# Kernel tuning notes

Measured on AMD Instinct MI355X. Metric: run time of the kernel, lower is better.

## Reference

```python
import jax, jax.numpy as jnp
import numpy as np

K = 100  # low-rank dimension


def setup_inputs() -> dict:
    key = jax.random.key(0)
    k1, k2 = jax.random.split(key)
    N, D = 100000, 512
    X = jax.random.normal(k1, (N, D), dtype=jnp.float32)
    # xavier-normal init for Linear(d, 4k): std = sqrt(2/(fan_in+fan_out))
    std = np.sqrt(2.0 / (D + 4 * K)).astype(np.float32)
    W = jax.random.normal(k2, (4 * K, D), dtype=jnp.float32) * std
    b = jnp.zeros((4 * K,), dtype=jnp.float32)
    return {"X": X, "W": W, "b": b}


def reference(X, W, b):
    # tmp = ReLU(X @ W^T + b): [N, 4k]
    tmp = jax.nn.relu(X @ W.T + b)
    U = tmp[:, :K]            # [N, k]
    V = tmp[:, K:2 * K]       # [N, k]
    Z = tmp[:, 2 * K:3 * K]   # [N, k]
    T = tmp[:, 3 * K:]        # [N, k]
    N_rows = X.shape[0]
    # joint_normalize2: sum(U @ (V^T @ ones)) / N + 1e-6 == <colsum(U), colsum(V)> / N + 1e-6
    norm_factor = jnp.dot(jnp.sum(U, axis=0), jnp.sum(V, axis=0)) / N_rows + 1e-6
    Dscale = 1.0 / norm_factor
    # low-rank attention: U @ (V^T @ Z) via small [k, k] intermediate
    VtZ = jnp.einsum('nk,nj->kj', V, Z)   # [k, k]
    res = (U @ VtZ) * Dscale              # [N, k]
    out = jnp.concatenate([res, T], axis=1)  # [N, 2k]
    # dropout p=0.0 (eval-equivalent): identity
    return out
```

## Files before the change

### kernel.cpp

```cpp
#include <hip/hip_runtime.h>
#include <cstdint>

typedef __bf16 bf16;
typedef __attribute__((ext_vector_type(8))) __bf16 bf16x8;
typedef __attribute__((ext_vector_type(4))) __bf16 bf16x4;
typedef __attribute__((ext_vector_type(4))) float f32x4;

#define NROWS 100000
#define DIM   512
#define NC    400
#define NBLK2 782

#define WS_WP    0u
#define WS_SUMU  458752u
#define WS_SUMV  459152u
#define WS_DSC   459552u
#define WS_VTZT  459776u
#define WS_U     524288u
#define WS_PART  66124288u
#define WS_SUMP  71041536u
#define WS_NEED  71667136u

__device__ __forceinline__ void gload_lds16(const void* g, void* l) {
  __builtin_amdgcn_global_load_lds(
      (const __attribute__((address_space(1))) uint32_t*)g,
      (__attribute__((address_space(3))) uint32_t*)l,
      16, 0, 0);
}

__global__ void k1_prep(const float* __restrict__ W, bf16* __restrict__ wp,
                        float* __restrict__ sums) {
  const int idx = blockIdx.x * 256 + threadIdx.x;
  if (idx < 200) sums[idx] = 0.f;
  if (idx >= 16 * 4 * 448 * 8) return;
  const int e = idx & 7;
  int r = idx >> 3;
  const int col = r % 448; r /= 448;
  const int g = r & 3;
  const int t = r >> 2;
  const int k = t * 32 + 4 * g + ((e < 4) ? e : (12 + e));
  wp[idx] = (bf16)((col < NC) ? W[col * DIM + k] : 0.f);
}

__global__ __launch_bounds__(512, 2) void k2_main(
    const float* __restrict__ X, const bf16* __restrict__ Wp,
    const float* __restrict__ bias, float* __restrict__ out,
    bf16* __restrict__ U, float* __restrict__ part, float* __restrict__ sumP) {
  __shared__ __align__(16) char pool[106496];
  char* Abase0 = pool;
  char* Bbase0 = pool + 49152;

  const int tid  = threadIdx.x;
  const int lane = tid & 63;
  const int wave = tid >> 6;
  const int wm = wave >> 2;
  const int wn = wave & 3;
  const int m  = lane & 15;
  const int g  = lane >> 4;
  const int rb = blockIdx.x * 128;

  f32x4 acc[4][7];
#pragma unroll
  for (int i = 0; i < 4; ++i)
#pragma unroll
    for (int j = 0; j < 7; ++j) acc[i][j] = (f32x4){0.f, 0.f, 0.f, 0.f};

  int gr0 = rb + wave * 16 + (lane >> 3);     if (gr0 > NROWS - 1) gr0 = NROWS - 1;
  int gr1 = rb + wave * 16 + 8 + (lane >> 3); if (gr1 > NROWS - 1) gr1 = NROWS - 1;
  const size_t swb = (size_t)(((lane & 7) ^ (lane >> 3)) * 16);
  const char* asrc0 = (const char*)X + (size_t)gr0 * 2048 + swb;
  const char* asrc1 = (const char*)X + (size_t)gr1 * 2048 + swb;
  const int bc0 = (wave < 4) ? wave * 4 : 16 + (wave - 4) * 3;
  const int nbc = (wave < 4) ? 4 : 3;
  const char* wpc = (const char*)Wp;

#define STAGE_A(T, BUF)                                                        \
  do {                                                                         \
    char* ad = Abase0 + (BUF) * 16384 + wave * 2048 + lane * 16;               \
    gload_lds16(asrc0 + (size_t)(T) * 128, ad);                                \
    gload_lds16(asrc1 + (size_t)(T) * 128, ad + 1024);                         \
  } while (0)
#define STAGE_B(T, BUF)                                                        \
  do {                                                                         \
    const char* bsrc = wpc + (size_t)(T) * 28672;                              \
    for (int q = 0; q < nbc; ++q)                                              \
      gload_lds16(bsrc + (bc0 + q) * 1024 + lane * 16,                         \
                  Bbase0 + (BUF) * 28672 + (bc0 + q) * 1024);                  \
  } while (0)

  STAGE_A(0, 0);
  STAGE_B(0, 0);
  STAGE_A(1, 1);

#pragma unroll
  for (int t = 0; t < 16; ++t) {
    const int ab  = t % 3;
    const int bb_ = t & 1;
    if (t < 15) STAGE_B(t + 1, bb_ ^ 1);
    if (t < 14) STAGE_A(t + 2, (t + 2) % 3);
    if (t < 14) {
      if (wave < 4) asm volatile("s_waitcnt vmcnt(8)\n\ts_barrier" ::: "memory");
      else          asm volatile("s_waitcnt vmcnt(7)\n\ts_barrier" ::: "memory");
    } else if (t == 14) {
      if (wave < 4) asm volatile("s_waitcnt vmcnt(6)\n\ts_barrier" ::: "memory");
      else          asm volatile("s_waitcnt vmcnt(5)\n\ts_barrier" ::: "memory");
    } else {
      asm volatile("s_waitcnt vmcnt(0)\n\ts_barrier" ::: "memory");
    }

    const int sw = (m & 7) * 16;
    const char* abuf = Abase0 + ab * 16384;
    bf16x8 af[4];
#pragma unroll
    for (int mf = 0; mf < 4; ++mf) {
      const char* rowp = abuf + (wm * 64 + mf * 16 + m) * 128;
      f32x4 alo = *(const f32x4*)(rowp + ((16 * g) ^ sw));
      f32x4 ahi = *(const f32x4*)(rowp + ((64 + 16 * g) ^ sw));
      af[mf] = (bf16x8){(bf16)alo.x, (bf16)alo.y, (bf16)alo.z, (bf16)alo.w,
                        (bf16)ahi.x, (bf16)ahi.y, (bf16)ahi.z, (bf16)ahi.w};
    }

    const bf16* Bc = (const bf16*)(Bbase0 + bb_ * 28672);
#pragma unroll
    for (int nf = 0; nf < 7; ++nf) {
      const int n = wn * 112 + nf * 16 + m;
      bf16x8 bfr = *(const bf16x8*)(Bc + (g * 448 + n) * 8);
#pragma unroll
      for (int mf = 0; mf < 4; ++mf)
        acc[mf][nf] = __builtin_amdgcn_mfma_f32_16x16x32_bf16(af[mf], bfr, acc[mf][nf], 0, 0, 0);
    }
    asm volatile("s_barrier" ::: "memory");
  }
#undef STAGE_A
#undef STAGE_B

  bf16* ldsVZ = (bf16*)pool;
  float* sp   = (float*)(pool + 61440);
  float csum[7];
#pragma unroll
  for (int nf = 0; nf < 7; ++nf) csum[nf] = 0.f;

#pragma unroll
  for (int mf = 0; mf < 4; ++mf) {
#pragma unroll
    for (int nf = 0; nf < 7; ++nf) {
      const int c = wn * 112 + nf * 16 + m;
      const float bv = (c < NC) ? bias[c] : 0.f;
#pragma unroll
      for (int r = 0; r < 4; ++r) {
        const int rl = wm * 64 + mf * 16 + 4 * g + r;
        const int row = rb + rl;
        float v = fmaxf(acc[mf][nf][r] + bv, 0.f);
        const float v2 = (row < NROWS) ? v : 0.f;
        if (row < NROWS) {
          if (c < 128) U[(size_t)row * 128 + c] = (c < 100) ? (bf16)v : (bf16)0.f;
          if (c >= 300 && c < NC) out[(size_t)row * 200 + 100 + (c - 300)] = v;
        }
        if (c >= 100 && c < 300)
          ldsVZ[(size_t)((c < 200) ? (c - 100) : (112 + (c - 200))) * 136 + rl] = (bf16)v2;
        if (c < 200) csum[nf] += v2;
      }
    }
  }
  for (int i = tid; i < 3264; i += 512) {
    const int q = i / 136, off = i % 136;
    const int lrow = (q < 12) ? (100 + q) : (200 + q);
    ldsVZ[lrow * 136 + off] = (bf16)0.f;
  }
#pragma unroll
  for (int nf = 0; nf < 7; ++nf) {
    float s = csum[nf];
    s += __shfl_xor(s, 16, 64);
    s += __shfl_xor(s, 32, 64);
    if (lane < 16) sp[wave * 112 + nf * 16 + lane] = s;
  }
  __syncthreads();

  if (wave < 7) {
    f32x4 acc2[7];
#pragma unroll
    for (int j = 0; j < 7; ++j) acc2[j] = (f32x4){0.f, 0.f, 0.f, 0.f};
    const bf16* vA = ldsVZ + (size_t)(wave * 16 + m) * 136;
#pragma unroll
    for (int kc = 0; kc < 4; ++kc) {
      bf16x4 a0 = *(const bf16x4*)(vA + kc * 32 + 4 * g);
      bf16x4 a1 = *(const bf16x4*)(vA + kc * 32 + 16 + 4 * g);
      bf16x8 af_ = {a0[0], a0[1], a0[2], a0[3], a1[0], a1[1], a1[2], a1[3]};
#pragma unroll
      for (int fj = 0; fj < 7; ++fj) {
        const bf16* vB = ldsVZ + (size_t)(112 + fj * 16 + m) * 136 + kc * 32;
        bf16x4 b0 = *(const bf16x4*)(vB + 4 * g);
        bf16x4 b1 = *(const bf16x4*)(vB + 16 + 4 * g);
        bf16x8 bf_ = {b0[0], b0[1], b0[2], b0[3], b1[0], b1[1], b1[2], b1[3]};
        acc2[fj] = __builtin_amdgcn_mfma_f32_16x16x32_bf16(af_, bf_, acc2[fj], 0, 0, 0);
      }
    }
    float* pb = part + (size_t)(blockIdx.x % 98) * 12544;
#pragma unroll
    for (int fj = 0; fj < 7; ++fj)
#pragma unroll
      for (int r = 0; r < 4; ++r)
        atomicAdd(&pb[(wave * 16 + 4 * g + r) * 112 + fj * 16 + m], acc2[fj][r]);
  }
  if (tid < 200) {
    const int wnc = tid / 112, cc = tid % 112;
    sumP[(size_t)blockIdx.x * 200 + tid] =
        sp[wnc * 112 + cc] + sp[(wnc + 4) * 112 + cc];
  }
}

__global__ void k4a0_redsum(const float* __restrict__ sumP,
                            float* __restrict__ sumU, float* __restrict__ sumV) {
  __shared__ float red[4];
  const int c = blockIdx.x;
  const int tid = threadIdx.x;
  float s = 0.f;
  for (int b = tid; b < NBLK2; b += 256) s += sumP[(size_t)b * 200 + c];
#pragma unroll
  for (int off = 1; off < 64; off <<= 1) s += __shfl_xor(s, off, 64);
  if ((tid & 63) == 0) red[tid >> 6] = s;
  __syncthreads();
  if (tid == 0) {
    float t = red[0] + red[1] + red[2] + red[3];
    if (c < 100) sumU[c] = t; else sumV[c - 100] = t;
  }
}

__global__ void k4a_norm(const float* __restrict__ sumU, const float* __restrict__ sumV,
                         float* __restrict__ dsc) {
  const int l = threadIdx.x;
  float v = 0.f;
  if (l < 50) v = sumU[l] * sumV[l] + sumU[l + 50] * sumV[l + 50];
#pragma unroll
  for (int off = 32; off > 0; off >>= 1) v += __shfl_down(v, off, 64);
  if (l == 0) dsc[0] = 1.f / (v * (1.f / (float)NROWS) + 1e-6f);
}

__global__ void k4b_final(const float* __restrict__ part, const float* __restrict__ dsc,
                          bf16* __restrict__ vtzt) {
  const int idx = blockIdx.x * 256 + threadIdx.x;
  if (idx < 1792) vtzt[(idx >> 4) * 128 + 112 + (idx & 15)] = (bf16)0.f;
  if (idx >= 12544) return;
  const int i = idx / 112;
  const int j = idx % 112;
  float s = 0.f;
#pragma unroll 7
  for (int bb = 0; bb < 98; ++bb) s += part[(size_t)bb * 12544 + idx];
  vtzt[j * 128 + i] = (bf16)(s * dsc[0]);
}

__global__ __launch_bounds__(256) void k5_res(
    const bf16* __restrict__ U, const bf16* __restrict__ vtzt,
    float* __restrict__ out) {
  const int tid = threadIdx.x;
  const int lane = tid & 63;
  const int wave = tid >> 6;
  const int m = lane & 15, g = lane >> 4;
  const int rb = blockIdx.x * 128 + wave * 32;

  f32x4 acc[2][7];
#pragma unroll
  for (int i = 0; i < 2; ++i)
#pragma unroll
    for (int j = 0; j < 7; ++j) acc[i][j] = (f32x4){0.f, 0.f, 0.f, 0.f};

  int r0 = rb + m;      if (r0 > NROWS - 1) r0 = NROWS - 1;
  int r1 = rb + 16 + m; if (r1 > NROWS - 1) r1 = NROWS - 1;
  const bf16* u0 = U + (size_t)r0 * 128 + 4 * g;
  const bf16* u1 = U + (size_t)r1 * 128 + 4 * g;
  const bf16* vb = vtzt + 4 * g;

#pragma unroll
  for (int ks = 0; ks < 4; ++ks) {
    bf16x4 A00 = *(const bf16x4*)(u0 + ks * 32);
    bf16x4 A01 = *(const bf16x4*)(u0 + ks * 32 + 16);
    bf16x4 A10 = *(const bf16x4*)(u1 + ks * 32);
    bf16x4 A11 = *(const bf16x4*)(u1 + ks * 32 + 16);
    bf16x8 af0 = {A00[0], A00[1], A00[2], A00[3], A01[0], A01[1], A01[2], A01[3]};
    bf16x8 af1 = {A10[0], A10[1], A10[2], A10[3], A11[0], A11[1], A11[2], A11[3]};
#pragma unroll
    for (int nf = 0; nf < 7; ++nf) {
      const int n = nf * 16 + m;
      bf16x4 B0 = *(const bf16x4*)(vb + n * 128 + ks * 32);
      bf16x4 B1 = *(const bf16x4*)(vb + n * 128 + ks * 32 + 16);
      bf16x8 bfr = {B0[0], B0[1], B0[2], B0[3], B1[0], B1[1], B1[2], B1[3]};
      acc[0][nf] = __builtin_amdgcn_mfma_f32_16x16x32_bf16(af0, bfr, acc[0][nf], 0, 0, 0);
      acc[1][nf] = __builtin_amdgcn_mfma_f32_16x16x32_bf16(af1, bfr, acc[1][nf], 0, 0, 0);
    }
  }
#pragma unroll
  for (int mf = 0; mf < 2; ++mf)
#pragma unroll
    for (int nf = 0; nf < 7; ++nf)
#pragma unroll
      for (int r = 0; r < 4; ++r) {
        const int row = rb + mf * 16 + 4 * g + r;
        const int c = nf * 16 + m;
        if (row < NROWS && c < 100)
          out[(size_t)row * 200 + c] = acc[mf][nf][r];
      }
}

extern "C" void kernel_launch(void* const* d_in, const int* in_sizes, int n_in,
                              void* d_out, int out_size, void* d_ws, size_t ws_size,
                              hipStream_t stream) {
  const float* X = (const float*)d_in[0];
  const float* W = (const float*)d_in[1];
  const float* b = (const float*)d_in[2];
  float* out = (float*)d_out;
  char* ws = (char*)d_ws;
  if (ws_size < WS_NEED) return;

  bf16* wp     = (bf16*)(ws + WS_WP);
  float* sumU  = (float*)(ws + WS_SUMU);
  float* sumV  = (float*)(ws + WS_SUMV);
  float* dsc   = (float*)(ws + WS_DSC);
  bf16* vtzt   = (bf16*)(ws + WS_VTZT);
  bf16* U      = (bf16*)(ws + WS_U);
  float* part  = (float*)(ws + WS_PART);
  float* sumP  = (float*)(ws + WS_SUMP);

  k1_prep<<<896, 256, 0, stream>>>(W, wp, sumU);
  hipMemsetAsync(part, 0, 98u * 12544u * 4u, stream);
  k2_main<<<NBLK2, 512, 0, stream>>>(X, wp, b, out, U, part, sumP);
  k4a0_redsum<<<200, 256, 0, stream>>>(sumP, sumU, sumV);
  k4a_norm<<<1, 64, 0, stream>>>(sumU, sumV, dsc);
  k4b_final<<<49, 256, 0, stream>>>(part, dsc, vtzt);
  k5_res<<<782, 256, 0, stream>>>(U, vtzt, out);
}
```

Before: 208.8 us.

## Split rows between LDS-staged kernel and a register-direct 64-row GEMM variant

Half the rows go through the existing LDS-staged 128-row kernel. The other half go through a new kernel that loads X directly into registers, converts it to bf16, and reads packed W fragments from global memory in 64-row blocks. The per-block V^T Z partials are split across two halves of the partial buffer, and the column-sum reduction is extended to cover both launches. The aim is to cut LDS staging overhead and raise occupancy, at the cost of repeated global W reads and an extra kernel launch.

```diff
diff --git a/kernel.cpp b/kernel.cpp
--- a/kernel.cpp
+++ b/kernel.cpp
@@ -9,7 +9,10 @@
 #define NROWS 100000
 #define DIM   512
 #define NC    400
-#define NBLK2 782
+#define NBLK_V0 391
+#define NBLK_V1 781
+#define ROW0_V1 50048
+#define NBLKTOT 1172
 
 #define WS_WP    0u
 #define WS_SUMU  458752u
@@ -19,7 +22,7 @@
 #define WS_U     524288u
 #define WS_PART  66124288u
 #define WS_SUMP  71041536u
-#define WS_NEED  71667136u
+#define WS_NEED  71979136u
 
 __device__ __forceinline__ void gload_lds16(const void* g, void* l) {
   __builtin_amdgcn_global_load_lds(
@@ -42,7 +45,7 @@
   wp[idx] = (bf16)((col < NC) ? W[col * DIM + k] : 0.f);
 }
 
-__global__ __launch_bounds__(512, 2) void k2_main(
+__global__ __launch_bounds__(512, 2) void k2_v0(
     const float* __restrict__ X, const bf16* __restrict__ Wp,
     const float* __restrict__ bias, float* __restrict__ out,
     bf16* __restrict__ U, float* __restrict__ part, float* __restrict__ sumP) {
@@ -195,7 +198,7 @@
         acc2[fj] = __builtin_amdgcn_mfma_f32_16x16x32_bf16(af_, bf_, acc2[fj], 0, 0, 0);
       }
     }
-    float* pb = part + (size_t)(blockIdx.x % 98) * 12544;
+    float* pb = part + (size_t)(blockIdx.x % 49) * 12544;
 #pragma unroll
     for (int fj = 0; fj < 7; ++fj)
 #pragma unroll
@@ -205,6 +208,127 @@
   if (tid < 200) {
     const int wnc = tid / 112, cc = tid % 112;
     sumP[(size_t)blockIdx.x * 200 + tid] =
+        sp[wnc * 112 + cc] + sp[(wnc + 4) * 112 + cc];
+  }
+}
+
+__global__ __launch_bounds__(512) void k2_v1(
+    const float* __restrict__ X, const bf16* __restrict__ Wp,
+    const float* __restrict__ bias, float* __restrict__ out,
+    bf16* __restrict__ U, float* __restrict__ part, float* __restrict__ sumP) {
+  __shared__ __align__(16) bf16 ldsVZ[224 * 72];
+  __shared__ float sp[8 * 112];
+
+  const int tid  = threadIdx.x;
+  const int lane = tid & 63;
+  const int wave = tid >> 6;
+  const int wm = wave >> 2;
+  const int wn = wave & 3;
+  const int m  = lane & 15;
+  const int g  = lane >> 4;
+  const int rbl = blockIdx.x * 64;
+  const int rb  = ROW0_V1 + rbl + wm * 32;
+
+  f32x4 acc[2][7];
+#pragma unroll
+  for (int i = 0; i < 2; ++i)
+#pragma unroll
+    for (int j = 0; j < 7; ++j) acc[i][j] = (f32x4){0.f, 0.f, 0.f, 0.f};
+
+  int r0 = rb + m;      if (r0 > NROWS - 1) r0 = NROWS - 1;
+  int r1 = rb + 16 + m; if (r1 > NROWS - 1) r1 = NROWS - 1;
+  const float* xp0 = X + (size_t)r0 * DIM + 4 * g;
+  const float* xp1 = X + (size_t)r1 * DIM + 4 * g;
+  const char* wb = (const char*)Wp + (size_t)(g * 448 + wn * 112 + m) * 16;
+
+#pragma unroll
+  for (int t = 0; t < 16; ++t) {
+    f32x4 a00 = *(const f32x4*)(xp0 + t * 32);
+    f32x4 a01 = *(const f32x4*)(xp0 + t * 32 + 16);
+    f32x4 a10 = *(const f32x4*)(xp1 + t * 32);
+    f32x4 a11 = *(const f32x4*)(xp1 + t * 32 + 16);
+    bf16x8 af0 = {(bf16)a00.x, (bf16)a00.y, (bf16)a00.z, (bf16)a00.w,
+                  (bf16)a01.x, (bf16)a01.y, (bf16)a01.z, (bf16)a01.w};
+    bf16x8 af1 = {(bf16)a10.x, (bf16)a10.y, (bf16)a10.z, (bf16)a10.w,
+                  (bf16)a11.x, (bf16)a11.y, (bf16)a11.z, (bf16)a11.w};
+    const char* wt = wb + (size_t)t * 28672;
+#pragma unroll
+    for (int nf = 0; nf < 7; ++nf) {
+      bf16x8 bfr = *(const bf16x8*)(wt + nf * 256);
+      acc[0][nf] = __builtin_amdgcn_mfma_f32_16x16x32_bf16(af0, bfr, acc[0][nf], 0, 0, 0);
+      acc[1][nf] = __builtin_amdgcn_mfma_f32_16x16x32_bf16(af1, bfr, acc[1][nf], 0, 0, 0);
+    }
+  }
+
+  float csum[7];
+#pragma unroll
+  for (int nf = 0; nf < 7; ++nf) csum[nf] = 0.f;
+
+#pragma unroll
+  for (int mf = 0; mf < 2; ++mf) {
+#pragma unroll
+    for (int nf = 0; nf < 7; ++nf) {
+      const int c = wn * 112 + nf * 16 + m;
+      const float bv = (c < NC) ? bias[c] : 0.f;
+#pragma unroll
+      for (int r = 0; r < 4; ++r) {
+        const int rl = wm * 32 + mf * 16 + 4 * g + r;
+        const int row = ROW0_V1 + rbl + rl;
+        float v = fmaxf(acc[mf][nf][r] + bv, 0.f);
+        const float v2 = (row < NROWS) ? v : 0.f;
+        if (row < NROWS) {
+          if (c < 128) U[(size_t)row * 128 + c] = (c < 100) ? (bf16)v : (bf16)0.f;
+          if (c >= 300 && c < NC) out[(size_t)row * 200 + 100 + (c - 300)] = v;
+        }
+        if (c >= 100 && c < 300)
+          ldsVZ[(size_t)((c < 200) ? (c - 100) : (112 + (c - 200))) * 72 + rl] = (bf16)v2;
+        if (c < 200) csum[nf] += v2;
+      }
+    }
+  }
+  for (int i = tid; i < 1728; i += 512) {
+    const int q = i / 72, off = i % 72;
+    const int lrow = (q < 12) ? (100 + q) : (200 + q);
+    ldsVZ[lrow * 72 + off] = (bf16)0.f;
+  }
+#pragma unroll
+  for (int nf = 0; nf < 7; ++nf) {
+    float s = csum[nf];
+    s += __shfl_xor(s, 16, 64);
+    s += __shfl_xor(s, 32, 64);
+    if (lane < 16) sp[wave * 112 + nf * 16 + lane] = s;
+  }
+  __syncthreads();
+
+  if (wave < 7) {
+    f32x4 acc2[7];
+#pragma unroll
+    for (int j = 0; j < 7; ++j) acc2[j] = (f32x4){0.f, 0.f, 0.f, 0.f};
+    const bf16* vA = ldsVZ + (size_t)(wave * 16 + m) * 72;
+#pragma unroll
+    for (int kc = 0; kc < 2; ++kc) {
+      bf16x4 a0 = *(const bf16x4*)(vA + kc * 32 + 4 * g);
+      bf16x4 a1 = *(const bf16x4*)(vA + kc * 32 + 16 + 4 * g);
+      bf16x8 af_ = {a0[0], a0[1], a0[2], a0[3], a1[0], a1[1], a1[2], a1[3]};
+#pragma unroll
+      for (int fj = 0; fj < 7; ++fj) {
+        const bf16* vB = ldsVZ + (size_t)(112 + fj * 16 + m) * 72 + kc * 32;
+        bf16x4 b0 = *(const bf16x4*)(vB + 4 * g);
+        bf16x4 b1 = *(const bf16x4*)(vB + 16 + 4 * g);
+        bf16x8 bf_ = {b0[0], b0[1], b0[2], b0[3], b1[0], b1[1], b1[2], b1[3]};
+        acc2[fj] = __builtin_amdgcn_mfma_f32_16x16x32_bf16(af_, bf_, acc2[fj], 0, 0, 0);
+      }
+    }
+    float* pb = part + (size_t)(49 + blockIdx.x % 49) * 12544;
+#pragma unroll
+    for (int fj = 0; fj < 7; ++fj)
+#pragma unroll
+      for (int r = 0; r < 4; ++r)
+        atomicAdd(&pb[(wave * 16 + 4 * g + r) * 112 + fj * 16 + m], acc2[fj][r]);
+  }
+  if (tid < 200) {
+    const int wnc = tid / 112, cc = tid % 112;
+    sumP[(size_t)(NBLK_V0 + blockIdx.x) * 200 + tid] =
         sp[wnc * 112 + cc] + sp[(wnc + 4) * 112 + cc];
   }
 }
@@ -215,7 +339,7 @@
   const int c = blockIdx.x;
   const int tid = threadIdx.x;
   float s = 0.f;
-  for (int b = tid; b < NBLK2; b += 256) s += sumP[(size_t)b * 200 + c];
+  for (int b = tid; b < NBLKTOT; b += 256) s += sumP[(size_t)b * 200 + c];
 #pragma unroll
   for (int off = 1; off < 64; off <<= 1) s += __shfl_xor(s, off, 64);
   if ((tid & 63) == 0) red[tid >> 6] = s;
@@ -322,7 +446,8 @@
 
   k1_prep<<<896, 256, 0, stream>>>(W, wp, sumU);
   hipMemsetAsync(part, 0, 98u * 12544u * 4u, stream);
-  k2_main<<<NBLK2, 512, 0, stream>>>(X, wp, b, out, U, part, sumP);
+  k2_v0<<<NBLK_V0, 512, 0, stream>>>(X, wp, b, out, U, part, sumP);
+  k2_v1<<<NBLK_V1, 512, 0, stream>>>(X, wp, b, out, U, part, sumP);
   k4a0_redsum<<<200, 256, 0, stream>>>(sumP, sumU, sumV);
   k4a_norm<<<1, 64, 0, stream>>>(sumU, sumV, dsc);
   k4b_final<<<49, 256, 0, stream>>>(part, dsc, vtzt);
```

Measured after the change: 271.9 us. 1.3x slower.

## Enlarge main GEMM block to 192 rows with 16 waves per block

Applied to the files above, without the earlier changes.

Retiles the fused GEMM kernel from 128-row blocks of 8 waves to 192-row blocks of 16 waves (1024 threads, 128 KB LDS), so each block stages the shared W tile once for more rows. This cuts the grid to 521 blocks and reduces the per-block VtZ partial MFMA and atomic work relative to rows processed. It also vectorises the V/Z LDS transposed stores into 4-element writes and drops the padding U writes for columns 100-127. In exchange it gives one block per CU with fewer accumulators per wave, lower occupancy flexibility, and a 4-wave-row reduction for column sums.

```diff
diff --git a/kernel.cpp b/kernel.cpp
--- a/kernel.cpp
+++ b/kernel.cpp
@@ -9,7 +9,7 @@
 #define NROWS 100000
 #define DIM   512
 #define NC    400
-#define NBLK2 782
+#define NBLK2 521
 
 #define WS_WP    0u
 #define WS_SUMU  458752u
@@ -19,7 +19,7 @@
 #define WS_U     524288u
 #define WS_PART  66124288u
 #define WS_SUMP  71041536u
-#define WS_NEED  71667136u
+#define WS_NEED  72291936u
 
 __device__ __forceinline__ void gload_lds16(const void* g, void* l) {
   __builtin_amdgcn_global_load_lds(
@@ -42,13 +42,13 @@
   wp[idx] = (bf16)((col < NC) ? W[col * DIM + k] : 0.f);
 }
 
-__global__ __launch_bounds__(512, 2) void k2_main(
+__global__ __launch_bounds__(1024) void k2_main(
     const float* __restrict__ X, const bf16* __restrict__ Wp,
     const float* __restrict__ bias, float* __restrict__ out,
     bf16* __restrict__ U, float* __restrict__ part, float* __restrict__ sumP) {
-  __shared__ __align__(16) char pool[106496];
+  __shared__ __align__(16) char pool[131072];
   char* Abase0 = pool;
-  char* Bbase0 = pool + 49152;
+  char* Bbase0 = pool + 73728;
 
   const int tid  = threadIdx.x;
   const int lane = tid & 63;
@@ -57,28 +57,30 @@
   const int wn = wave & 3;
   const int m  = lane & 15;
   const int g  = lane >> 4;
-  const int rb = blockIdx.x * 128;
-
-  f32x4 acc[4][7];
-#pragma unroll
-  for (int i = 0; i < 4; ++i)
+  const int rb = blockIdx.x * 192;
+
+  f32x4 acc[3][7];
+#pragma unroll
+  for (int i = 0; i < 3; ++i)
 #pragma unroll
     for (int j = 0; j < 7; ++j) acc[i][j] = (f32x4){0.f, 0.f, 0.f, 0.f};
 
-  int gr0 = rb + wave * 16 + (lane >> 3);     if (gr0 > NROWS - 1) gr0 = NROWS - 1;
-  int gr1 = rb + wave * 16 + 8 + (lane >> 3); if (gr1 > NROWS - 1) gr1 = NROWS - 1;
+  const int nba = (wave < 8) ? 2 : 1;
+  const int ca0 = (wave < 8) ? wave * 2 : 16 + (wave - 8);
   const size_t swb = (size_t)(((lane & 7) ^ (lane >> 3)) * 16);
+  int gr0 = rb + ca0 * 8 + (lane >> 3);       if (gr0 > NROWS - 1) gr0 = NROWS - 1;
+  int gr1 = rb + (ca0 + 1) * 8 + (lane >> 3); if (gr1 > NROWS - 1) gr1 = NROWS - 1;
   const char* asrc0 = (const char*)X + (size_t)gr0 * 2048 + swb;
   const char* asrc1 = (const char*)X + (size_t)gr1 * 2048 + swb;
-  const int bc0 = (wave < 4) ? wave * 4 : 16 + (wave - 4) * 3;
-  const int nbc = (wave < 4) ? 4 : 3;
+  const int nbc = (wave < 12) ? 2 : 1;
+  const int bc0 = (wave < 12) ? wave * 2 : 24 + (wave - 12);
   const char* wpc = (const char*)Wp;
 
 #define STAGE_A(T, BUF)                                                        \
   do {                                                                         \
-    char* ad = Abase0 + (BUF) * 16384 + wave * 2048 + lane * 16;               \
+    char* ad = Abase0 + (BUF) * 24576 + ca0 * 1024 + lane * 16;                \
     gload_lds16(asrc0 + (size_t)(T) * 128, ad);                                \
-    gload_lds16(asrc1 + (size_t)(T) * 128, ad + 1024);                         \
+    if (nba == 2) gload_lds16(asrc1 + (size_t)(T) * 128, ad + 1024);           \
   } while (0)
 #define STAGE_B(T, BUF)                                                        \
   do {                                                                         \
@@ -99,21 +101,23 @@
     if (t < 15) STAGE_B(t + 1, bb_ ^ 1);
     if (t < 14) STAGE_A(t + 2, (t + 2) % 3);
     if (t < 14) {
-      if (wave < 4) asm volatile("s_waitcnt vmcnt(8)\n\ts_barrier" ::: "memory");
-      else          asm volatile("s_waitcnt vmcnt(7)\n\ts_barrier" ::: "memory");
+      if (wave < 8)       asm volatile("s_waitcnt vmcnt(6)\n\ts_barrier" ::: "memory");
+      else if (wave < 12) asm volatile("s_waitcnt vmcnt(4)\n\ts_barrier" ::: "memory");
+      else                asm volatile("s_waitcnt vmcnt(3)\n\ts_barrier" ::: "memory");
     } else if (t == 14) {
-      if (wave < 4) asm volatile("s_waitcnt vmcnt(6)\n\ts_barrier" ::: "memory");
-      else          asm volatile("s_waitcnt vmcnt(5)\n\ts_barrier" ::: "memory");
+      if (wave < 8)       asm volatile("s_waitcnt vmcnt(4)\n\ts_barrier" ::: "memory");
+      else if (wave < 12) asm volatile("s_waitcnt vmcnt(3)\n\ts_barrier" ::: "memory");
+      else                asm volatile("s_waitcnt vmcnt(2)\n\ts_barrier" ::: "memory");
     } else {
       asm volatile("s_waitcnt vmcnt(0)\n\ts_barrier" ::: "memory");
     }
 
     const int sw = (m & 7) * 16;
-    const char* abuf = Abase0 + ab * 16384;
-    bf16x8 af[4];
-#pragma unroll
-    for (int mf = 0; mf < 4; ++mf) {
-      const char* rowp = abuf + (wm * 64 + mf * 16 + m) * 128;
+    const char* abuf = Abase0 + ab * 24576;
+    bf16x8 af[3];
+#pragma unroll
+    for (int mf = 0; mf < 3; ++mf) {
+      const char* rowp = abuf + (wm * 48 + mf * 16 + m) * 128;
       f32x4 alo = *(const f32x4*)(rowp + ((16 * g) ^ sw));
       f32x4 ahi = *(const f32x4*)(rowp + ((64 + 16 * g) ^ sw));
       af[mf] = (bf16x8){(bf16)alo.x, (bf16)alo.y, (bf16)alo.z, (bf16)alo.w,
@@ -126,7 +130,7 @@
       const int n = wn * 112 + nf * 16 + m;
       bf16x8 bfr = *(const bf16x8*)(Bc + (g * 448 + n) * 8);
 #pragma unroll
-      for (int mf = 0; mf < 4; ++mf)
+      for (int mf = 0; mf < 3; ++mf)
         acc[mf][nf] = __builtin_amdgcn_mfma_f32_16x16x32_bf16(af[mf], bfr, acc[mf][nf], 0, 0, 0);
     }
     asm volatile("s_barrier" ::: "memory");
@@ -135,37 +139,40 @@
 #undef STAGE_B
 
   bf16* ldsVZ = (bf16*)pool;
-  float* sp   = (float*)(pool + 61440);
+  float* sp   = (float*)(pool + 89600);
   float csum[7];
 #pragma unroll
   for (int nf = 0; nf < 7; ++nf) csum[nf] = 0.f;
 
 #pragma unroll
-  for (int mf = 0; mf < 4; ++mf) {
+  for (int mf = 0; mf < 3; ++mf) {
 #pragma unroll
     for (int nf = 0; nf < 7; ++nf) {
       const int c = wn * 112 + nf * 16 + m;
       const float bv = (c < NC) ? bias[c] : 0.f;
+      const int rl0 = wm * 48 + mf * 16 + 4 * g;
+      bf16 vz[4];
 #pragma unroll
       for (int r = 0; r < 4; ++r) {
-        const int rl = wm * 64 + mf * 16 + 4 * g + r;
-        const int row = rb + rl;
+        const int row = rb + rl0 + r;
         float v = fmaxf(acc[mf][nf][r] + bv, 0.f);
         const float v2 = (row < NROWS) ? v : 0.f;
         if (row < NROWS) {
-          if (c < 128) U[(size_t)row * 128 + c] = (c < 100) ? (bf16)v : (bf16)0.f;
+          if (c < 100) U[(size_t)row * 128 + c] = (bf16)v;
           if (c >= 300 && c < NC) out[(size_t)row * 200 + 100 + (c - 300)] = v;
         }
-        if (c >= 100 && c < 300)
-          ldsVZ[(size_t)((c < 200) ? (c - 100) : (112 + (c - 200))) * 136 + rl] = (bf16)v2;
+        vz[r] = (bf16)v2;
         if (c < 200) csum[nf] += v2;
       }
-    }
-  }
-  for (int i = tid; i < 3264; i += 512) {
-    const int q = i / 136, off = i % 136;
-    const int lrow = (q < 12) ? (100 + q) : (200 + q);
-    ldsVZ[lrow * 136 + off] = (bf16)0.f;
+      if (c >= 100 && c < 300) {
+        const int vr = (c < 200) ? (c - 100) : (112 + (c - 200));
+        *(bf16x4*)&ldsVZ[(size_t)vr * 200 + rl0] = (bf16x4){vz[0], vz[1], vz[2], vz[3]};
+      }
+    }
+  }
+  for (int i = tid; i < 4800; i += 1024) {
+    const int rr = (i < 2400) ? (100 + i / 200) : (212 + (i - 2400) / 200);
+    ldsVZ[(size_t)rr * 200 + (i % 200)] = (bf16)0.f;
   }
 #pragma unroll
   for (int nf = 0; nf < 7; ++nf) {
@@ -180,15 +187,15 @@
     f32x4 acc2[7];
 #pragma unroll
     for (int j = 0; j < 7; ++j) acc2[j] = (f32x4){0.f, 0.f, 0.f, 0.f};
-    const bf16* vA = ldsVZ + (size_t)(wave * 16 + m) * 136;
-#pragma unroll
-    for (int kc = 0; kc < 4; ++kc) {
+    const bf16* vA = ldsVZ + (size_t)(wave * 16 + m) * 200;
+#pragma unroll
+    for (int kc = 0; kc < 6; ++kc) {
       bf16x4 a0 = *(const bf16x4*)(vA + kc * 32 + 4 * g);
       bf16x4 a1 = *(const bf16x4*)(vA + kc * 32 + 16 + 4 * g);
       bf16x8 af_ = {a0[0], a0[1], a0[2], a0[3], a1[0], a1[1], a1[2], a1[3]};
 #pragma unroll
       for (int fj = 0; fj < 7; ++fj) {
-        const bf16* vB = ldsVZ + (size_t)(112 + fj * 16 + m) * 136 + kc * 32;
+        const bf16* vB = ldsVZ + (size_t)(112 + fj * 16 + m) * 200 + kc * 32;
         bf16x4 b0 = *(const bf16x4*)(vB + 4 * g);
         bf16x4 b1 = *(const bf16x4*)(vB + 16 + 4 * g);
         bf16x8 bf_ = {b0[0], b0[1], b0[2], b0[3], b1[0], b1[1], b1[2], b1[3]};
@@ -203,9 +210,10 @@
         atomicAdd(&pb[(wave * 16 + 4 * g + r) * 112 + fj * 16 + m], acc2[fj][r]);
   }
   if (tid < 200) {
-    const int wnc = tid / 112, cc = tid % 112;
+    const int wq = tid / 112, cc = tid % 112;
     sumP[(size_t)blockIdx.x * 200 + tid] =
-        sp[wnc * 112 + cc] + sp[(wnc + 4) * 112 + cc];
+        sp[(0 * 4 + wq) * 112 + cc] + sp[(1 * 4 + wq) * 112 + cc] +
+        sp[(2 * 4 + wq) * 112 + cc] + sp[(3 * 4 + wq) * 112 + cc];
   }
 }
 
@@ -322,7 +330,7 @@
 
   k1_prep<<<896, 256, 0, stream>>>(W, wp, sumU);
   hipMemsetAsync(part, 0, 98u * 12544u * 4u, stream);
-  k2_main<<<NBLK2, 512, 0, stream>>>(X, wp, b, out, U, part, sumP);
+  k2_main<<<NBLK2, 1024, 0, stream>>>(X, wp, b, out, U, part, sumP);
   k4a0_redsum<<<200, 256, 0, stream>>>(sumP, sumU, sumV);
   k4a_norm<<<1, 64, 0, stream>>>(sumU, sumV, dsc);
   k4b_final<<<49, 256, 0, stream>>>(part, dsc, vtzt);
```

New measurement: 208.8 us. About the same (-0.0%).

## Triple-buffer A and B tiles with one barrier per k-step and MFMA priority

Applied to the files above, without the earlier changes.

Reworks the GEMM main loop so the A and B operand tiles share one triple-buffered ring. The next-next stage is issued after a single waitcnt+barrier, which removes the trailing per-iteration barrier. s_setprio raises wave priority around the MFMA block so compute issues ahead of memory traffic. The epilogue packs four V/Z bf16 values into one vectorised LDS store and skips writing the zero padding columns of U. LDS grows from 104 KB to 132 KB, which may break the 2-blocks-per-CU occupancy target. U's padding columns 100-127 are no longer zeroed, so correctness depends on whether later code reads them.

```diff
diff --git a/kernel.cpp b/kernel.cpp
--- a/kernel.cpp
+++ b/kernel.cpp
@@ -46,7 +46,7 @@
     const float* __restrict__ X, const bf16* __restrict__ Wp,
     const float* __restrict__ bias, float* __restrict__ out,
     bf16* __restrict__ U, float* __restrict__ part, float* __restrict__ sumP) {
-  __shared__ __align__(16) char pool[106496];
+  __shared__ __align__(16) char pool[135168];
   char* Abase0 = pool;
   char* Bbase0 = pool + 49152;
 
@@ -74,42 +74,33 @@
   const int nbc = (wave < 4) ? 4 : 3;
   const char* wpc = (const char*)Wp;
 
-#define STAGE_A(T, BUF)                                                        \
+#define STAGE(T, BUF)                                                          \
   do {                                                                         \
     char* ad = Abase0 + (BUF) * 16384 + wave * 2048 + lane * 16;               \
     gload_lds16(asrc0 + (size_t)(T) * 128, ad);                                \
     gload_lds16(asrc1 + (size_t)(T) * 128, ad + 1024);                         \
-  } while (0)
-#define STAGE_B(T, BUF)                                                        \
-  do {                                                                         \
     const char* bsrc = wpc + (size_t)(T) * 28672;                              \
     for (int q = 0; q < nbc; ++q)                                              \
       gload_lds16(bsrc + (bc0 + q) * 1024 + lane * 16,                         \
                   Bbase0 + (BUF) * 28672 + (bc0 + q) * 1024);                  \
   } while (0)
 
-  STAGE_A(0, 0);
-  STAGE_B(0, 0);
-  STAGE_A(1, 1);
+  STAGE(0, 0);
+  STAGE(1, 1);
 
 #pragma unroll
   for (int t = 0; t < 16; ++t) {
-    const int ab  = t % 3;
-    const int bb_ = t & 1;
-    if (t < 15) STAGE_B(t + 1, bb_ ^ 1);
-    if (t < 14) STAGE_A(t + 2, (t + 2) % 3);
-    if (t < 14) {
-      if (wave < 4) asm volatile("s_waitcnt vmcnt(8)\n\ts_barrier" ::: "memory");
-      else          asm volatile("s_waitcnt vmcnt(7)\n\ts_barrier" ::: "memory");
-    } else if (t == 14) {
+    const int cur = t % 3;
+    if (t < 15) {
       if (wave < 4) asm volatile("s_waitcnt vmcnt(6)\n\ts_barrier" ::: "memory");
       else          asm volatile("s_waitcnt vmcnt(5)\n\ts_barrier" ::: "memory");
     } else {
       asm volatile("s_waitcnt vmcnt(0)\n\ts_barrier" ::: "memory");
     }
+    if (t + 2 < 16) STAGE(t + 2, (t + 2) % 3);
 
     const int sw = (m & 7) * 16;
-    const char* abuf = Abase0 + ab * 16384;
+    const char* abuf = Abase0 + cur * 16384;
     bf16x8 af[4];
 #pragma unroll
     for (int mf = 0; mf < 4; ++mf) {
@@ -120,7 +111,8 @@
                         (bf16)ahi.x, (bf16)ahi.y, (bf16)ahi.z, (bf16)ahi.w};
     }
 
-    const bf16* Bc = (const bf16*)(Bbase0 + bb_ * 28672);
+    const bf16* Bc = (const bf16*)(Bbase0 + cur * 28672);
+    __builtin_amdgcn_s_setprio(1);
 #pragma unroll
     for (int nf = 0; nf < 7; ++nf) {
       const int n = wn * 112 + nf * 16 + m;
@@ -129,10 +121,10 @@
       for (int mf = 0; mf < 4; ++mf)
         acc[mf][nf] = __builtin_amdgcn_mfma_f32_16x16x32_bf16(af[mf], bfr, acc[mf][nf], 0, 0, 0);
     }
-    asm volatile("s_barrier" ::: "memory");
-  }
-#undef STAGE_A
-#undef STAGE_B
+    __builtin_amdgcn_s_setprio(0);
+  }
+#undef STAGE
+  __syncthreads();
 
   bf16* ldsVZ = (bf16*)pool;
   float* sp   = (float*)(pool + 61440);
@@ -146,19 +138,23 @@
     for (int nf = 0; nf < 7; ++nf) {
       const int c = wn * 112 + nf * 16 + m;
       const float bv = (c < NC) ? bias[c] : 0.f;
+      const int rl0 = wm * 64 + mf * 16 + 4 * g;
+      bf16 vz[4];
 #pragma unroll
       for (int r = 0; r < 4; ++r) {
-        const int rl = wm * 64 + mf * 16 + 4 * g + r;
-        const int row = rb + rl;
+        const int row = rb + rl0 + r;
         float v = fmaxf(acc[mf][nf][r] + bv, 0.f);
         const float v2 = (row < NROWS) ? v : 0.f;
         if (row < NROWS) {
-          if (c < 128) U[(size_t)row * 128 + c] = (c < 100) ? (bf16)v : (bf16)0.f;
+          if (c < 100) U[(size_t)row * 128 + c] = (bf16)v;
           if (c >= 300 && c < NC) out[(size_t)row * 200 + 100 + (c - 300)] = v;
         }
-        if (c >= 100 && c < 300)
-          ldsVZ[(size_t)((c < 200) ? (c - 100) : (112 + (c - 200))) * 136 + rl] = (bf16)v2;
+        vz[r] = (bf16)v2;
         if (c < 200) csum[nf] += v2;
+      }
+      if (c >= 100 && c < 300) {
+        const int vr = (c < 200) ? (c - 100) : (112 + (c - 200));
+        *(bf16x4*)&ldsVZ[(size_t)vr * 136 + rl0] = (bf16x4){vz[0], vz[1], vz[2], vz[3]};
       }
     }
   }
```

Measured after the change: 200.4 us. 4.0% less time.
